# Optimization experiments

Hardware: AMD Instinct MI355X
Metric: run time of the kernel (lower is better)

Reference implementation:

```python
import jax, jax.numpy as jnp
import numpy as np

DEGREE_RES = 15
NUM_ROT = int(np.ceil(360 / DEGREE_RES))  # 24
PIXEL_SIZE = 0.0625
IM_METERS = 4.0
IM_SIZE = int(IM_METERS / PIXEL_SIZE)  # 64


def _create_rot_mat():
    angles = np.radians([i * DEGREE_RES for i in range(NUM_ROT)])
    c, s = np.cos(angles), np.sin(angles)
    rot = np.stack([
        np.stack([c, np.zeros_like(c), -s], axis=-1),
        np.stack([np.zeros_like(c), np.ones_like(c), np.zeros_like(c)], axis=-1),
        np.stack([s, np.zeros_like(c), c], axis=-1),
    ], axis=1)  # [NUM_ROT, 3, 3]
    return jnp.asarray(rot, dtype=jnp.float32)


def setup_inputs() -> dict:
    key = jax.random.key(0)
    xyz = jax.random.normal(key, (32, 16384, 3), dtype=jnp.float32)
    rot_mat = _create_rot_mat()
    return {"xyz": xyz, "rot_mat": rot_mat}


def reference(xyz, rot_mat):
    B, N, _ = xyz.shape
    R = rot_mat.shape[0]
    # rotate each point by each rotation: [B, R, N, 3]
    xyz_rot = jnp.einsum('rij,bnj->brni', rot_mat, xyz)
    # project x,z -> pixel indices (offset by half image extent, 2 meters)
    proj = jnp.round((xyz_rot[..., :2] + IM_METERS / 2) / PIXEL_SIZE).astype(jnp.int32)
    mask = ((proj[..., 0] >= 0) & (proj[..., 0] < IM_SIZE) &
            (proj[..., 1] >= 0) & (proj[..., 1] < IM_SIZE))
    # out-of-range points are zeroed -> they (faithfully) write at pixel (0,0)
    proj = proj * mask[..., None]
    vals = xyz_rot[..., 2] / 10.0  # non-occupancy branch: scatter z/10
    image = jnp.zeros((B, R, IM_SIZE, IM_SIZE), dtype=xyz.dtype)
    b = jnp.arange(B)[:, None, None]
    r = jnp.arange(R)[None, :, None]
    image = image.at[b, r, proj[..., 1], proj[..., 0]].set(vals)
    return image
```

## Files before the change

### kernel.cpp

```cpp
#include <hip/hip_runtime.h>
#include <stdint.h>

#define BB 32
#define NN 16384
#define RR 24
#define IMS 64
#define NPIX (IMS * IMS)
#define TOTAL_PIX (BB * RR * NPIX)

__global__ __launch_bounds__(1024, 8) void rotproj_lds(
    const float* __restrict__ xyz, const float* __restrict__ rot,
    float* __restrict__ out) {
  __shared__ unsigned int img[NPIX];

  const int blk = blockIdx.x;
  const int b = blk / RR;
  const int r = blk - b * RR;

  for (int i = threadIdx.x; i < NPIX; i += 1024) img[i] = 0u;

  const float* m = rot + r * 9;
  const float m0 = m[0], m2 = m[2], m6 = m[6], m8 = m[8];

  __syncthreads();

  const float4* base4 = (const float4*)(xyz + (size_t)b * NN * 3);
  const int lane = threadIdx.x & 63;

#pragma unroll
  for (int iter = 0; iter < 2; ++iter) {
    const int n0 = iter * 8192 + threadIdx.x * 8;
    const int v = 6 * (n0 >> 3);
    const float4 f0 = base4[v + 0];
    const float4 f1 = base4[v + 1];
    const float4 f2 = base4[v + 2];
    const float4 f3 = base4[v + 3];
    const float4 f4 = base4[v + 4];
    const float4 f5 = base4[v + 5];

    const float xs[8] = {f0.x, f0.w, f1.z, f2.y, f3.x, f3.w, f4.z, f5.y};
    const float ys[8] = {f0.y, f1.x, f1.w, f2.z, f3.y, f4.x, f4.w, f5.z};
    const float zs[8] = {f0.z, f1.y, f2.x, f2.w, f3.z, f4.y, f5.x, f5.w};

    bool anyoob = false;
    unsigned int oobkey = 0u;

#pragma unroll
    for (int j = 0; j < 8; ++j) {
      const float x = xs[j], y = ys[j], z = zs[j];

      const float xr = __fadd_rn(__fmul_rn(m0, x), __fmul_rn(m2, z));
      const float zr = __fadd_rn(__fmul_rn(m6, x), __fmul_rn(m8, z));

      const int px = (int)rintf(__fmaf_rn(xr, 16.0f, 32.0f));
      const int py = (int)rintf(__fmaf_rn(y, 16.0f, 32.0f));
      const bool in = ((unsigned)px < (unsigned)IMS) &
                      ((unsigned)py < (unsigned)IMS);

      const unsigned int key = ((unsigned)(n0 + j + 1) << 17) |
                               (__float_as_uint(zr) >> 15);

      if (in) {
        atomicMax(&img[py * IMS + px], key);
      } else {
        anyoob = true;
        oobkey = key;
      }
    }

    const unsigned long long oob = __ballot(anyoob);
    if (anyoob && lane == 63 - __builtin_clzll(oob)) {
      atomicMax(&img[0], oobkey);
    }
  }

  __syncthreads();

  float* oslice = out + (size_t)blk * NPIX;
#pragma unroll
  for (int t = 0; t < 4; ++t) {
    const int i = t * 1024 + threadIdx.x;
    const unsigned int k = img[i];
    const float zr = __uint_as_float((k & 0x1FFFFu) << 15);
    oslice[i] = k ? (zr / 10.0f) : 0.0f;
  }
}

extern "C" void kernel_launch(void* const* d_in, const int* in_sizes, int n_in,
                              void* d_out, int out_size, void* d_ws,
                              size_t ws_size, hipStream_t stream) {
  const float* xyz = (const float*)d_in[0];
  const float* rot = (const float*)d_in[1];
  float* out = (float*)d_out;

  rotproj_lds<<<BB * RR, 1024, 0, stream>>>(xyz, rot, out);
}
```

Before: 70.58 us.

## Process three rotations per block to reuse loaded points across images

Each block now builds three rotation images in LDS instead of one, so each batch's point cloud is read once per three rotations rather than once per rotation. The grid shrinks from 768 to 256 blocks, LDS per block triples to 48KB, and per-point work (y projection, key base) is shared across rotations. The cost is fewer blocks to fill the GPU's CUs and lower occupancy from the larger LDS footprint.

```diff
diff --git a/kernel.cpp b/kernel.cpp
--- a/kernel.cpp
+++ b/kernel.cpp
@@ -6,21 +6,30 @@
 #define RR 24
 #define IMS 64
 #define NPIX (IMS * IMS)
+#define RPB 3
+#define GROUPS (RR / RPB)
 #define TOTAL_PIX (BB * RR * NPIX)
 
-__global__ __launch_bounds__(1024, 8) void rotproj_lds(
+__global__ __launch_bounds__(1024) void rotproj_lds(
     const float* __restrict__ xyz, const float* __restrict__ rot,
     float* __restrict__ out) {
-  __shared__ unsigned int img[NPIX];
+  __shared__ unsigned int img[RPB * NPIX];
 
   const int blk = blockIdx.x;
-  const int b = blk / RR;
-  const int r = blk - b * RR;
+  const int b = blk >> 3;
+  const int rg = blk & (GROUPS - 1);
 
-  for (int i = threadIdx.x; i < NPIX; i += 1024) img[i] = 0u;
+  for (int i = threadIdx.x; i < RPB * NPIX; i += 1024) img[i] = 0u;
 
-  const float* m = rot + r * 9;
-  const float m0 = m[0], m2 = m[2], m6 = m[6], m8 = m[8];
+  const float* m = rot + rg * RPB * 9;
+  float c0[RPB], c2[RPB], c6[RPB], c8[RPB];
+#pragma unroll
+  for (int rl = 0; rl < RPB; ++rl) {
+    c0[rl] = m[rl * 9 + 0];
+    c2[rl] = m[rl * 9 + 2];
+    c6[rl] = m[rl * 9 + 6];
+    c8[rl] = m[rl * 9 + 8];
+  }
 
   __syncthreads();
 
@@ -42,43 +51,52 @@
     const float ys[8] = {f0.y, f1.x, f1.w, f2.z, f3.y, f4.x, f4.w, f5.z};
     const float zs[8] = {f0.z, f1.y, f2.x, f2.w, f3.z, f4.y, f5.x, f5.w};
 
-    bool anyoob = false;
-    unsigned int oobkey = 0u;
+    bool anyoob[RPB] = {false, false, false};
+    unsigned int oobkey[RPB] = {0u, 0u, 0u};
 
 #pragma unroll
     for (int j = 0; j < 8; ++j) {
       const float x = xs[j], y = ys[j], z = zs[j];
 
-      const float xr = __fadd_rn(__fmul_rn(m0, x), __fmul_rn(m2, z));
-      const float zr = __fadd_rn(__fmul_rn(m6, x), __fmul_rn(m8, z));
+      const int py = (int)rintf(__fmaf_rn(y, 16.0f, 32.0f));
+      const bool pyin = (unsigned)py < (unsigned)IMS;
+      const unsigned int nkey = (unsigned)(n0 + j + 1) << 17;
 
-      const int px = (int)rintf(__fmaf_rn(xr, 16.0f, 32.0f));
-      const int py = (int)rintf(__fmaf_rn(y, 16.0f, 32.0f));
-      const bool in = ((unsigned)px < (unsigned)IMS) &
-                      ((unsigned)py < (unsigned)IMS);
+#pragma unroll
+      for (int rl = 0; rl < RPB; ++rl) {
+        const float xr =
+            __fadd_rn(__fmul_rn(c0[rl], x), __fmul_rn(c2[rl], z));
+        const float zr =
+            __fadd_rn(__fmul_rn(c6[rl], x), __fmul_rn(c8[rl], z));
 
-      const unsigned int key = ((unsigned)(n0 + j + 1) << 17) |
-                               (__float_as_uint(zr) >> 15);
+        const int px = (int)rintf(__fmaf_rn(xr, 16.0f, 32.0f));
+        const bool in = ((unsigned)px < (unsigned)IMS) & pyin;
 
-      if (in) {
-        atomicMax(&img[py * IMS + px], key);
-      } else {
-        anyoob = true;
-        oobkey = key;
+        const unsigned int key = nkey | (__float_as_uint(zr) >> 15);
+
+        if (in) {
+          atomicMax(&img[rl * NPIX + py * IMS + px], key);
+        } else {
+          anyoob[rl] = true;
+          oobkey[rl] = key;
+        }
       }
     }
 
-    const unsigned long long oob = __ballot(anyoob);
-    if (anyoob && lane == 63 - __builtin_clzll(oob)) {
-      atomicMax(&img[0], oobkey);
+#pragma unroll
+    for (int rl = 0; rl < RPB; ++rl) {
+      const unsigned long long oob = __ballot(anyoob[rl]);
+      if (anyoob[rl] && lane == 63 - __builtin_clzll(oob)) {
+        atomicMax(&img[rl * NPIX], oobkey[rl]);
+      }
     }
   }
 
   __syncthreads();
 
-  float* oslice = out + (size_t)blk * NPIX;
+  float* oslice = out + ((size_t)b * RR + (size_t)rg * RPB) * NPIX;
 #pragma unroll
-  for (int t = 0; t < 4; ++t) {
+  for (int t = 0; t < RPB * NPIX / 1024; ++t) {
     const int i = t * 1024 + threadIdx.x;
     const unsigned int k = img[i];
     const float zr = __uint_as_float((k & 0x1FFFFu) << 15);
@@ -93,5 +111,5 @@
   const float* rot = (const float*)d_in[1];
   float* out = (float*)d_out;
 
-  rotproj_lds<<<BB * RR, 1024, 0, stream>>>(xyz, rot, out);
+  rotproj_lds<<<BB * GROUPS, 1024, 0, stream>>>(xyz, rot, out);
 }
```

Result: no change. 70.36 us (-0.3%).
